# Performance work log

Hardware: AMD Instinct MI355X
Metric: run time of the kernel (lower is better)

Reference implementation:

```python
import jax, jax.numpy as jnp
import numpy as np
import math

LMAX = 10
N_SH = (LMAX + 1) ** 2  # 121
_lambert_sh_k = [3.1415926535897927, 2.0943951023931957, 0.7853981633974483, 0.0,
                 -0.13089969389957473, 0.0, 0.04908738521234052, 0.0,
                 -0.024543692606170262, 0.0, 0.014317154020265985]
_reps = [2 * l + 1 for l in range(LMAX + 1)]
LAMBERT_VEC = jnp.asarray(np.repeat(np.array(_lambert_sh_k, np.float32), _reps))  # (121,)
EXPO_VEC = jnp.asarray(np.repeat(np.array([l * (l + 1) / 2.0 for l in range(LMAX + 1)], np.float32), _reps))  # (121,)

def _dfact(n):
    # double factorial n!!, with (-1)!! = 1
    out = 1.0
    while n > 0:
        out *= n
        n -= 2
    return out

def _K(l, m):
    return math.sqrt((2 * l + 1) / (4 * math.pi) * math.factorial(l - m) / math.factorial(l + m))

def sh_basis(d):
    """Real spherical harmonics up to LMAX, e3nn-style ordering (m=-l..l per l),
    'integral' normalization, homogeneous in |d| (normalize=False semantics: Y_l(r*u)=r^l Y_l(u))."""
    r = jnp.linalg.norm(d, axis=-1, keepdims=True)  # (N,1)
    u = d / jnp.maximum(r, 1e-12)
    x, y, z = u[..., 0], u[..., 1], u[..., 2]
    rr = r[..., 0]
    # c[m] = sin^m(theta)*cos(m*phi), s[m] = sin^m(theta)*sin(m*phi) via complex power recurrence
    c = [jnp.ones_like(x)]
    s = [jnp.zeros_like(x)]
    for m in range(1, LMAX + 1):
        c.append(x * c[m - 1] - y * s[m - 1])
        s.append(x * s[m - 1] + y * c[m - 1])
    # Q[l][m] = P_l^m(z) / sin^m(theta) (polynomial in z, no Condon-Shortley)
    Q = {}
    for m in range(LMAX + 1):
        Q[(m, m)] = jnp.full_like(x, _dfact(2 * m - 1))
        if m < LMAX:
            Q[(m + 1, m)] = (2 * m + 1) * z * Q[(m, m)]
        for l in range(m + 2, LMAX + 1):
            Q[(l, m)] = ((2 * l - 1) * z * Q[(l - 1, m)] - (l + m - 1) * Q[(l - 2, m)]) / (l - m)
    cols = [None] * N_SH
    for l in range(LMAX + 1):
        rl = rr ** l
        cols[l * l + l] = _K(l, 0) * Q[(l, 0)] * rl
        for m in range(1, l + 1):
            f = math.sqrt(2.0) * _K(l, m)
            cols[l * l + l + m] = f * Q[(l, m)] * c[m] * rl
            cols[l * l + l - m] = f * Q[(l, m)] * s[m] * rl
    return jnp.stack(cols, axis=-1)  # (N, 121)

def setup_inputs() -> dict:
    key = jax.random.key(0)
    ks = jax.random.split(key, 16)
    N = 131072
    W = 512
    normals = jax.random.normal(ks[0], (N, 3), jnp.float32)
    normals = normals / jnp.linalg.norm(normals, axis=-1, keepdims=True)
    view_dirs = jax.random.normal(ks[1], (N, 3), jnp.float32)
    view_dirs = view_dirs / jnp.linalg.norm(view_dirs, axis=-1, keepdims=True)
    feature = jax.random.normal(ks[2], (N, 16), jnp.float32)
    ref_SH = jax.random.normal(ks[3], (N, N_SH, 3), jnp.float32) * 0.1
    def xavier(k, fi, fo):
        lim = math.sqrt(6.0 / (fi + fo))
        return jax.random.uniform(k, (fi, fo), jnp.float32, -lim, lim)
    return {
        'normals': normals, 'view_dirs': view_dirs, 'feature': feature, 'ref_SH': ref_SH,
        'w0': xavier(ks[4], 8, W), 'b0': jnp.zeros((W,), jnp.float32),
        'w1': xavier(ks[5], W, W), 'b1': jnp.zeros((W,), jnp.float32),
        'w2': xavier(ks[6], W, W), 'b2': jnp.zeros((W,), jnp.float32),
        'w3': xavier(ks[7], W, W), 'b3': jnp.zeros((W,), jnp.float32),
        'wc': xavier(ks[8], W, 27), 'bc': jnp.zeros((27,), jnp.float32),
    }

def reference(normals, view_dirs, feature, ref_SH, w0, b0, w1, b1, w2, b2, w3, b3, wc, bc):
    roughness = jax.nn.softplus(feature[..., 0:1])          # (N,1)
    coe = feature[..., 1:10]                                 # (N,9)
    albedo = jax.nn.sigmoid(feature[..., 10:13])             # (N,3)
    spec = jax.nn.sigmoid(feature[..., 13:16])               # (N,3)
    # diffuse irradiance: Lambert-coefficient-weighted SH of normals
    irradiance = jax.nn.relu(jnp.einsum('nk,nkc->nc', sh_basis(normals) * LAMBERT_VEC, ref_SH))
    diffuse = albedo * irradiance
    # specular: roughness-filtered SH of reflection direction
    dot = jnp.sum(normals * view_dirs, axis=-1, keepdims=True)  # (N,1)
    wr = 2.0 * normals * dot - view_dirs                        # (N,3)
    decay = jnp.exp(-EXPO_VEC * roughness)                      # (N,121)
    light = jax.nn.relu(jnp.einsum('nk,nkc->nc', sh_basis(wr) * decay, ref_SH))
    # conditioning MLP
    h = jnp.concatenate([dot, view_dirs, normals, roughness], axis=-1)  # (N,8)
    h = jax.nn.relu(h @ w0 + b0)
    h = jax.nn.relu(h @ w1 + b1)
    h = jax.nn.relu(h @ w2 + b2)
    h = jax.nn.relu(h @ w3 + b3)
    cs = h @ wc + bc                                            # (N,27)
    rr_ = jnp.sum(cs[..., 0:9] * coe, axis=-1, keepdims=True)
    gg_ = jnp.sum(cs[..., 9:18] * coe, axis=-1, keepdims=True)
    bb_ = jnp.sum(cs[..., 18:27] * coe, axis=-1, keepdims=True)
    gate = jax.nn.sigmoid(jnp.concatenate([rr_, gg_, bb_], axis=-1))  # (N,3)
    specular = spec * light * gate
    raw_rgb = diffuse + specular
    sh_light = jnp.concatenate([light, irradiance], axis=0)     # (2N,3)
    return raw_rgb, albedo, diffuse, specular, sh_light
```

## Files before the change

### kernel.cpp

```cpp
#include <hip/hip_runtime.h>
#include <hip/hip_bf16.h>
#include <stdint.h>
#include <math.h>

typedef __hip_bfloat16 bf16;
typedef __attribute__((ext_vector_type(8))) __bf16 bf16x8;
typedef __attribute__((ext_vector_type(4))) float f32x4;

__device__ __forceinline__ float b2f(bf16 x){ return __bfloat162float(x); }
__device__ __forceinline__ bf16 f2b(float x){ return __float2bfloat16(x); }
__device__ __forceinline__ float sigmoidf_(float x){ return 1.f/(1.f+expf(-x)); }

__device__ __forceinline__ void ld_lds16(const void* g, void* l){
  __builtin_amdgcn_global_load_lds(
      (const __attribute__((address_space(1))) uint32_t*)g,
      (__attribute__((address_space(3))) uint32_t*)l, 16, 0, 0);
}

__device__ const float DTAB[11] = {1.f,1.f,3.f,15.f,105.f,945.f,10395.f,135135.f,
                                   2027025.f,34459425.f,654729075.f};
__device__ const float LAMB[11] = {3.1415926535897927f, 2.0943951023931957f, 0.7853981633974483f,
                                   0.0f, -0.13089969389957473f, 0.0f, 0.04908738521234052f, 0.0f,
                                   -0.024543692606170262f, 0.0f, 0.014317154020265985f};

__global__ __launch_bounds__(256) void transpose512(const float* __restrict__ w1,
                                                    const float* __restrict__ w2,
                                                    const float* __restrict__ w3,
                                                    bf16* __restrict__ outT){
  __shared__ float tile[64][65];
  const float* src = (blockIdx.z==0) ? w1 : (blockIdx.z==1) ? w2 : w3;
  bf16* dst = outT + (size_t)blockIdx.z*512*512;
  int bx = blockIdx.x*64, by = blockIdx.y*64;
  int tx = threadIdx.x & 63, tg = threadIdx.x >> 6;
  #pragma unroll
  for (int rr=0; rr<16; rr++){
    int row = tg*16 + rr;
    tile[row][tx] = src[(by+row)*512 + bx+tx];
  }
  __syncthreads();
  #pragma unroll
  for (int rr=0; rr<16; rr++){
    int row = tg*16 + rr;
    dst[(size_t)(bx+row)*512 + by+tx] = f2b(tile[tx][row]);
  }
}

__global__ __launch_bounds__(256) void prep_wcT(const float* __restrict__ wc, bf16* __restrict__ wcT){
  int i = blockIdx.x*256 + threadIdx.x;
  int n = i >> 9, k = i & 511;
  wcT[i] = f2b((n < 27) ? wc[k*27 + n] : 0.f);
}

__global__ __launch_bounds__(256) void prep_small(const float* b0, const float* b1,
    const float* b2, const float* b3, const float* bc, const float* w0,
    float* __restrict__ fsm){
  int i = blockIdx.x*256 + threadIdx.x;
  if (i >= 6176) return;
  float v;
  if (i < 512)       v = b0[i];
  else if (i < 1024) v = b1[i-512];
  else if (i < 1536) v = b2[i-1024];
  else if (i < 2048) v = b3[i-1536];
  else if (i < 2080){ int j=i-2048; v = (j<27) ? bc[j] : 0.f; }
  else               v = w0[i-2080];
  fsm[i] = v;
}

__global__ __launch_bounds__(256) void point_kernel(
    const float* __restrict__ nrm, const float* __restrict__ vwd,
    const float* __restrict__ feat, const float* __restrict__ refsh,
    float* __restrict__ out, float* __restrict__ lightirr, float* __restrict__ h0, int N)
{
  __shared__ float rows[32*363];
  __shared__ float s_klm[66];
  const int tid = threadIdx.x;
  if (tid < 66){
    int l = 0, t = tid;
    while (t >= l+1){ t -= (l+1); l++; }
    int m = t;
    double fr = 1.0;
    for (int i = l-m+1; i <= l+m; i++) fr /= (double)i;
    double K = sqrt((2.0*l+1.0)/(4.0*3.14159265358979323846) * fr);
    if (m > 0) K *= 1.4142135623730951;
    s_klm[tid] = (float)K;
  }
  const int wave = tid >> 6, lane = tid & 63;
  const long p0 = (long)blockIdx.x * 32;
  const float* gbase = refsh + p0*363;
  #pragma unroll
  for (int t=0; t<12; t++){
    int fi = t*1024 + wave*256 + lane*4;
    if (fi < 32*363)
      ld_lds16(gbase + fi, rows + t*1024 + wave*256);
  }
  __syncthreads();

  const int r = tid >> 3, j = tid & 7;
  const long p = p0 + r;
  const float* row = rows + r*363;

  float nx=nrm[p*3+0], ny=nrm[p*3+1], nz=nrm[p*3+2];
  float vx=vwd[p*3+0], vy=vwd[p*3+1], vz=vwd[p*3+2];
  float f0 = feat[p*16];
  float rough = (f0 > 20.f) ? f0 : log1pf(expf(f0));
  float dotnv = nx*vx + ny*vy + nz*vz;
  float wx = 2.f*nx*dotnv - vx, wy = 2.f*ny*dotnv - vy, wz = 2.f*nz*dotnv - vz;

  float rA = sqrtf(nx*nx+ny*ny+nz*nz);
  float iA = 1.f/fmaxf(rA, 1e-12f);
  float ax = nx*iA, ay = ny*iA, az = nz*iA;
  float rB = sqrtf(wx*wx+wy*wy+wz*wz);
  float iB = 1.f/fmaxf(rB, 1e-12f);
  float bx = wx*iB, by = wy*iB, bz = wz*iB;

  float irr[3] = {0,0,0}, lig[3] = {0,0,0};
  const float E = expf(-rough);

  auto process_m = [&](int m){
    float cmA=1.f, smA=0.f, cmB=1.f, smB=0.f, rmA=1.f, rmB=1.f;
    for (int mm=1; mm<=m; mm++){
      float tA = ax*cmA - ay*smA; smA = ax*smA + ay*cmA; cmA = tA;
      float tB = bx*cmB - by*smB; smB = bx*smB + by*cmB; cmB = tB;
      rmA *= rA; rmB *= rB;
    }
    float qA = DTAB[m], qB = DTAB[m], pA = 0.f, pB = 0.f;
    float rlA = rmA, rlB = rmB;
    float dec = expf(-0.5f*(float)(m*(m+1))*rough);
    float e   = expf(-(float)(m+1)*rough);
    for (int l=m; l<=10; l++){
      if (l > m){
        float nA, nB;
        if (l == m+1){ nA = (float)(2*m+1)*az*qA; nB = (float)(2*m+1)*bz*qB; }
        else {
          float inv = 1.f/(float)(l-m);
          nA = ((float)(2*l-1)*az*qA - (float)(l+m-1)*pA)*inv;
          nB = ((float)(2*l-1)*bz*qB - (float)(l+m-1)*pB)*inv;
        }
        pA = qA; qA = nA; pB = qB; qB = nB;
        rlA *= rA; rlB *= rB;
        dec *= e; e *= E;
      }
      float kc = s_klm[l*(l+1)/2 + m];
      float wI = kc*qA*rlA*LAMB[l];
      float wL = kc*qB*rlB*dec;
      int k0 = l*l + l;
      if (m == 0){
        const float* rp = row + k0*3;
        #pragma unroll
        for (int c=0;c<3;c++){ float rv = rp[c]; irr[c] += wI*rv; lig[c] += wL*rv; }
      } else {
        const float* rpp = row + (k0+m)*3;
        const float* rpm = row + (k0-m)*3;
        #pragma unroll
        for (int c=0;c<3;c++){ float rv = rpp[c]; irr[c] += wI*cmA*rv; lig[c] += wL*cmB*rv; }
        #pragma unroll
        for (int c=0;c<3;c++){ float rv = rpm[c]; irr[c] += wI*smA*rv; lig[c] += wL*smB*rv; }
      }
    }
  };
  process_m(j);
  if (j < 3) process_m(j+8);

  #pragma unroll
  for (int c=0;c<3;c++){
    #pragma unroll
    for (int s=4; s>=1; s>>=1){
      irr[c] += __shfl_xor(irr[c], s);
      lig[c] += __shfl_xor(lig[c], s);
    }
  }
  float ir[3], lg[3];
  #pragma unroll
  for (int c=0;c<3;c++){ ir[c] = fmaxf(irr[c],0.f); lg[c] = fmaxf(lig[c],0.f); }

  long N3 = (long)3*N;
  if (j < 3){
    int c = j;
    float alb = sigmoidf_(feat[p*16+10+c]);
    out[N3   + p*3 + c] = alb;
    out[2*N3 + p*3 + c] = alb*ir[c];
    out[4*N3 + p*3 + c] = lg[c];
    out[4*N3 + ((long)N+p)*3 + c] = ir[c];
  }
  if (j < 6) lightirr[p*6 + j] = (j<3) ? lg[j] : ir[j-3];
  float hv = (j==0)?dotnv : (j==1)?vx : (j==2)?vy : (j==3)?vz :
             (j==4)?nx   : (j==5)?ny : (j==6)?nz : rough;
  h0[p*8 + j] = hv;
}

__global__ __launch_bounds__(256) void gemm0(const float* __restrict__ h0,
    const float* __restrict__ w0f, const float* __restrict__ b0f,
    bf16* __restrict__ outp, int rows){
  __shared__ float w0s[8*512];
  __shared__ float b0s[512];
  int tid = threadIdx.x;
  #pragma unroll
  for (int i=0;i<16;i++){ int e = i*256+tid; w0s[e] = w0f[e]; }
  b0s[tid] = b0f[tid]; b0s[256+tid] = b0f[256+tid];
  __syncthreads();
  long r = (long)blockIdx.x*32 + (tid>>3);
  int cg = tid & 7;
  float hv[8];
  #pragma unroll
  for (int k=0;k<8;k++) hv[k] = h0[r*8+k];
  bf16* orow = outp + r*512;
  for (int cc=0; cc<64; cc++){
    int col = cg + cc*8;
    float a = b0s[col];
    #pragma unroll
    for (int k=0;k<8;k++) a += hv[k]*w0s[k*512+col];
    orow[col] = f2b(fmaxf(a, 0.f));
  }
}

template<int WN, bool RELU, bool OUTBF>
__global__ __launch_bounds__(256) void gemm_bt(
    const bf16* __restrict__ A, const bf16* __restrict__ Bt,
    const float* __restrict__ bias,
    void* __restrict__ outv, int ldout, int rows)
{
  constexpr int BN = 32*WN;
  constexpr int BK = 64;
  constexpr int NCH_B = BN/32;
  __shared__ bf16 As[128*BK];
  __shared__ bf16 Bs[BN*BK];
  const int tid  = threadIdx.x;
  const int wave = tid >> 6, lane = tid & 63;
  const int quad = lane >> 4, l16 = lane & 15;
  const int wrow = wave >> 1, wcol = wave & 1;
  const int m_off = wrow*64, n_off = wcol*16*WN;
  const long rowBase = (long)blockIdx.x * 128;
  const int  colBase = blockIdx.y * BN;

  f32x4 acc[4][WN];
  #pragma unroll
  for (int i=0;i<4;i++)
    #pragma unroll
    for (int j=0;j<WN;j++) acc[i][j] = (f32x4){0.f,0.f,0.f,0.f};

  for (int kt=0; kt<512; kt+=BK){
    #pragma unroll
    for (int ch=0; ch<4; ch++){
      int flat = ch*2048 + wave*512 + lane*8;
      int m = flat >> 6, kk = flat & 63;
      ld_lds16(A + (rowBase + m)*512 + kt + kk, As + ch*2048 + wave*512);
    }
    #pragma unroll
    for (int ch=0; ch<NCH_B; ch++){
      int flat = ch*2048 + wave*512 + lane*8;
      int n = flat >> 6, kk = flat & 63;
      ld_lds16(Bt + (long)(colBase + n)*512 + kt + kk, Bs + ch*2048 + wave*512);
    }
    __syncthreads();
    #pragma unroll
    for (int kk=0; kk<BK; kk+=32){
      bf16x8 af[4], bfr[WN];
      #pragma unroll
      for (int i=0;i<4;i++)
        af[i] = *(const bf16x8*)(As + (m_off + i*16 + l16)*BK + kk + quad*8);
      #pragma unroll
      for (int j=0;j<WN;j++)
        bfr[j] = *(const bf16x8*)(Bs + (n_off + j*16 + l16)*BK + kk + quad*8);
      #pragma unroll
      for (int i=0;i<4;i++)
        #pragma unroll
        for (int j=0;j<WN;j++)
          acc[i][j] = __builtin_amdgcn_mfma_f32_16x16x32_bf16(af[i], bfr[j], acc[i][j], 0,0,0);
    }
    __syncthreads();
  }
  #pragma unroll
  for (int j=0;j<WN;j++){
    int cg = colBase + n_off + j*16 + l16;
    float bv = bias[cg];
    #pragma unroll
    for (int i=0;i<4;i++){
      long rg0 = rowBase + m_off + i*16 + quad*4;
      #pragma unroll
      for (int r=0;r<4;r++){
        float v = acc[i][j][r] + bv;
        if (RELU) v = fmaxf(v, 0.f);
        if (OUTBF) ((bf16*)outv)[(rg0+r)*(long)ldout + cg] = f2b(v);
        else       ((float*)outv)[(rg0+r)*(long)ldout + cg] = v;
      }
    }
  }
}

__global__ __launch_bounds__(256) void epilogue_kernel(const float* __restrict__ cs,
    const float* __restrict__ feat, const float* __restrict__ lightirr,
    float* __restrict__ out, long base, int N, int rows){
  int t = blockIdx.x*256 + threadIdx.x;
  if (t >= rows) return;
  long gp = base + t;
  const float* c = cs + (long)t*32;
  const float* f = feat + gp*16;
  float rr=0.f, gg=0.f, bb=0.f;
  #pragma unroll
  for (int j=0;j<9;j++){
    float co = f[1+j];
    rr += c[j]*co; gg += c[9+j]*co; bb += c[18+j]*co;
  }
  float gate[3] = { sigmoidf_(rr), sigmoidf_(gg), sigmoidf_(bb) };
  const float* li = lightirr + gp*6;
  long N3 = (long)3*N;
  #pragma unroll
  for (int cc=0; cc<3; cc++){
    float spec = sigmoidf_(f[13+cc]);
    float alb  = sigmoidf_(f[10+cc]);
    float specular = spec * li[cc] * gate[cc];
    float diffuse  = alb * li[3+cc];
    out[gp*3 + cc]        = diffuse + specular;
    out[3*N3 + gp*3 + cc] = specular;
  }
}

extern "C" void kernel_launch(void* const* d_in, const int* in_sizes, int n_in,
                              void* d_out, int out_size, void* d_ws, size_t ws_size,
                              hipStream_t stream) {
  const float* normals = (const float*)d_in[0];
  const float* viewd   = (const float*)d_in[1];
  const float* feat    = (const float*)d_in[2];
  const float* refsh   = (const float*)d_in[3];
  float* out = (float*)d_out;
  int N = in_sizes[0] / 3;

  char* ws = (char*)d_ws;
  size_t off = 0;
  bf16* wT  = (bf16*)(ws + off);            off += (size_t)3*512*512*2;
  bf16* wcT = (bf16*)(ws + off);            off += (size_t)32*512*2;
  float* fsm = (float*)(ws + off);          off += (size_t)6176*4; off = (off+255)&~(size_t)255;
  float* h0 = (float*)(ws + off);           off += (size_t)N*8*4;
  float* lightirr = (float*)(ws + off);     off += (size_t)N*6*4;
  size_t fixed = off;

  size_t avail = (ws_size > fixed) ? (ws_size - fixed) : 0;
  long chunk = (long)(avail / 2176) & ~255L;
  if (chunk < 256) chunk = 256;
  if (chunk > N) chunk = N;
  bf16* hA = (bf16*)(ws + fixed);
  bf16* hB = (bf16*)(ws + fixed + (size_t)chunk*1024);
  float* cs = (float*)(ws + fixed + (size_t)chunk*2048);

  transpose512<<<dim3(8,8,3), 256, 0, stream>>>((const float*)d_in[6], (const float*)d_in[8],
                                                (const float*)d_in[10], wT);
  prep_wcT<<<64, 256, 0, stream>>>((const float*)d_in[12], wcT);
  prep_small<<<25, 256, 0, stream>>>((const float*)d_in[5], (const float*)d_in[7],
                                     (const float*)d_in[9], (const float*)d_in[11],
                                     (const float*)d_in[13], (const float*)d_in[4], fsm);
  point_kernel<<<N/32, 256, 0, stream>>>(normals, viewd, feat, refsh, out, lightirr, h0, N);

  for (long base = 0; base < N; base += chunk){
    long rows = (N - base < chunk) ? (N - base) : chunk;
    gemm0<<<rows/32, 256, 0, stream>>>(h0 + base*8, fsm + 2080, fsm + 0, hA, (int)rows);
    gemm_bt<4,true,true ><<<dim3(rows/128,4), 256, 0, stream>>>(hA, wT,          fsm + 512,  hB, 512, (int)rows);
    gemm_bt<4,true,true ><<<dim3(rows/128,4), 256, 0, stream>>>(hB, wT + 262144, fsm + 1024, hA, 512, (int)rows);
    gemm_bt<4,true,true ><<<dim3(rows/128,4), 256, 0, stream>>>(hA, wT + 524288, fsm + 1536, hB, 512, (int)rows);
    gemm_bt<1,false,false><<<dim3(rows/128,1), 256, 0, stream>>>(hB, wcT,        fsm + 2048, cs,  32, (int)rows);
    epilogue_kernel<<<rows/256, 256, 0, stream>>>(cs, feat, lightirr, out, base, N, (int)rows);
  }
}
```

Before: 801.6 us.

## Swizzle LDS layout in GEMMs and fuse head GEMM with gate epilogue

```diff
diff --git a/kernel.cpp b/kernel.cpp
--- a/kernel.cpp
+++ b/kernel.cpp
@@ -213,64 +213,63 @@
   }
 }
 
-template<int WN, bool RELU, bool OUTBF>
+
 __global__ __launch_bounds__(256) void gemm_bt(
     const bf16* __restrict__ A, const bf16* __restrict__ Bt,
-    const float* __restrict__ bias,
-    void* __restrict__ outv, int ldout, int rows)
+    const float* __restrict__ bias, bf16* __restrict__ outp, int rows)
 {
-  constexpr int BN = 32*WN;
   constexpr int BK = 64;
-  constexpr int NCH_B = BN/32;
   __shared__ bf16 As[128*BK];
-  __shared__ bf16 Bs[BN*BK];
+  __shared__ bf16 Bs[128*BK];
   const int tid  = threadIdx.x;
   const int wave = tid >> 6, lane = tid & 63;
   const int quad = lane >> 4, l16 = lane & 15;
   const int wrow = wave >> 1, wcol = wave & 1;
-  const int m_off = wrow*64, n_off = wcol*16*WN;
+  const int m_off = wrow*64, n_off = wcol*64;
   const long rowBase = (long)blockIdx.x * 128;
-  const int  colBase = blockIdx.y * BN;
-
-  f32x4 acc[4][WN];
+  const int  colBase = blockIdx.y * 128;
+  const int sw = (lane&7) ^ ((lane>>3)&7);
+  const int rowlow = lane >> 3;
+
+  f32x4 acc[4][4];
   #pragma unroll
   for (int i=0;i<4;i++)
     #pragma unroll
-    for (int j=0;j<WN;j++) acc[i][j] = (f32x4){0.f,0.f,0.f,0.f};
+    for (int j=0;j<4;j++) acc[i][j] = (f32x4){0.f,0.f,0.f,0.f};
 
   for (int kt=0; kt<512; kt+=BK){
     #pragma unroll
     for (int ch=0; ch<4; ch++){
-      int flat = ch*2048 + wave*512 + lane*8;
-      int m = flat >> 6, kk = flat & 63;
-      ld_lds16(A + (rowBase + m)*512 + kt + kk, As + ch*2048 + wave*512);
-    }
-    #pragma unroll
-    for (int ch=0; ch<NCH_B; ch++){
-      int flat = ch*2048 + wave*512 + lane*8;
-      int n = flat >> 6, kk = flat & 63;
-      ld_lds16(Bt + (long)(colBase + n)*512 + kt + kk, Bs + ch*2048 + wave*512);
+      int m = ch*32 + wave*8 + rowlow;
+      ld_lds16(A + (rowBase + m)*512 + kt + sw*8, As + ch*2048 + wave*512);
+      int n = ch*32 + wave*8 + rowlow;
+      ld_lds16(Bt + (long)(colBase + n)*512 + kt + sw*8, Bs + ch*2048 + wave*512);
     }
     __syncthreads();
     #pragma unroll
     for (int kk=0; kk<BK; kk+=32){
-      bf16x8 af[4], bfr[WN];
-      #pragma unroll
-      for (int i=0;i<4;i++)
-        af[i] = *(const bf16x8*)(As + (m_off + i*16 + l16)*BK + kk + quad*8);
-      #pragma unroll
-      for (int j=0;j<WN;j++)
-        bfr[j] = *(const bf16x8*)(Bs + (n_off + j*16 + l16)*BK + kk + quad*8);
+      const int kb = kk >> 3;
+      bf16x8 af[4], bfr[4];
+      #pragma unroll
+      for (int i=0;i<4;i++){
+        int row = m_off + i*16 + l16;
+        af[i] = *(const bf16x8*)(As + row*BK + (((kb+quad) ^ (row&7))<<3));
+      }
+      #pragma unroll
+      for (int j=0;j<4;j++){
+        int row = n_off + j*16 + l16;
+        bfr[j] = *(const bf16x8*)(Bs + row*BK + (((kb+quad) ^ (row&7))<<3));
+      }
       #pragma unroll
       for (int i=0;i<4;i++)
         #pragma unroll
-        for (int j=0;j<WN;j++)
+        for (int j=0;j<4;j++)
           acc[i][j] = __builtin_amdgcn_mfma_f32_16x16x32_bf16(af[i], bfr[j], acc[i][j], 0,0,0);
     }
     __syncthreads();
   }
   #pragma unroll
-  for (int j=0;j<WN;j++){
+  for (int j=0;j<4;j++){
     int cg = colBase + n_off + j*16 + l16;
     float bv = bias[cg];
     #pragma unroll
@@ -278,40 +277,99 @@
       long rg0 = rowBase + m_off + i*16 + quad*4;
       #pragma unroll
       for (int r=0;r<4;r++){
-        float v = acc[i][j][r] + bv;
-        if (RELU) v = fmaxf(v, 0.f);
-        if (OUTBF) ((bf16*)outv)[(rg0+r)*(long)ldout + cg] = f2b(v);
-        else       ((float*)outv)[(rg0+r)*(long)ldout + cg] = v;
-      }
-    }
-  }
-}
-
-__global__ __launch_bounds__(256) void epilogue_kernel(const float* __restrict__ cs,
+        float v = fmaxf(acc[i][j][r] + bv, 0.f);
+        outp[(rg0+r)*512 + cg] = f2b(v);
+      }
+    }
+  }
+}
+
+__global__ __launch_bounds__(256) void head_gate(
+    const bf16* __restrict__ A, const bf16* __restrict__ wcT,
+    const float* __restrict__ bcp,
     const float* __restrict__ feat, const float* __restrict__ lightirr,
-    float* __restrict__ out, long base, int N, int rows){
-  int t = blockIdx.x*256 + threadIdx.x;
-  if (t >= rows) return;
-  long gp = base + t;
-  const float* c = cs + (long)t*32;
-  const float* f = feat + gp*16;
-  float rr=0.f, gg=0.f, bb=0.f;
-  #pragma unroll
-  for (int j=0;j<9;j++){
-    float co = f[1+j];
-    rr += c[j]*co; gg += c[9+j]*co; bb += c[18+j]*co;
-  }
-  float gate[3] = { sigmoidf_(rr), sigmoidf_(gg), sigmoidf_(bb) };
-  const float* li = lightirr + gp*6;
-  long N3 = (long)3*N;
-  #pragma unroll
-  for (int cc=0; cc<3; cc++){
-    float spec = sigmoidf_(f[13+cc]);
-    float alb  = sigmoidf_(f[10+cc]);
-    float specular = spec * li[cc] * gate[cc];
-    float diffuse  = alb * li[3+cc];
-    out[gp*3 + cc]        = diffuse + specular;
-    out[3*N3 + gp*3 + cc] = specular;
+    float* __restrict__ out, long base, int N)
+{
+  constexpr int BK = 64;
+  __shared__ bf16 As[128*BK];
+  __shared__ bf16 Bs[32*BK];
+  __shared__ float scs[128*33];
+  const int tid  = threadIdx.x;
+  const int wave = tid >> 6, lane = tid & 63;
+  const int quad = lane >> 4, l16 = lane & 15;
+  const int wrow = wave >> 1, wcol = wave & 1;
+  const int m_off = wrow*64, n_off = wcol*16;
+  const long rowBase = (long)blockIdx.x * 128;
+  const int sw = (lane&7) ^ ((lane>>3)&7);
+  const int rowlow = lane >> 3;
+
+  f32x4 acc[4];
+  #pragma unroll
+  for (int i=0;i<4;i++) acc[i] = (f32x4){0.f,0.f,0.f,0.f};
+
+  for (int kt=0; kt<512; kt+=BK){
+    #pragma unroll
+    for (int ch=0; ch<4; ch++){
+      int m = ch*32 + wave*8 + rowlow;
+      ld_lds16(A + (rowBase + m)*512 + kt + sw*8, As + ch*2048 + wave*512);
+    }
+    {
+      int n = wave*8 + rowlow;
+      ld_lds16(wcT + (long)n*512 + kt + sw*8, Bs + wave*512);
+    }
+    __syncthreads();
+    #pragma unroll
+    for (int kk=0; kk<BK; kk+=32){
+      const int kb = kk >> 3;
+      bf16x8 af[4], bfr;
+      #pragma unroll
+      for (int i=0;i<4;i++){
+        int row = m_off + i*16 + l16;
+        af[i] = *(const bf16x8*)(As + row*BK + (((kb+quad) ^ (row&7))<<3));
+      }
+      {
+        int row = n_off + l16;
+        bfr = *(const bf16x8*)(Bs + row*BK + (((kb+quad) ^ (row&7))<<3));
+      }
+      #pragma unroll
+      for (int i=0;i<4;i++)
+        acc[i] = __builtin_amdgcn_mfma_f32_16x16x32_bf16(af[i], bfr, acc[i], 0,0,0);
+    }
+    __syncthreads();
+  }
+  {
+    int cg = n_off + l16;
+    float bv = bcp[cg];
+    #pragma unroll
+    for (int i=0;i<4;i++){
+      int r0 = m_off + i*16 + quad*4;
+      #pragma unroll
+      for (int r=0;r<4;r++)
+        scs[(r0+r)*33 + cg] = acc[i][r] + bv;
+    }
+  }
+  __syncthreads();
+  if (tid < 128){
+    long gp = base + rowBase + tid;
+    const float* f = feat + gp*16;
+    const float* c = scs + tid*33;
+    float rr=0.f, gg=0.f, bb=0.f;
+    #pragma unroll
+    for (int j=0;j<9;j++){
+      float co = f[1+j];
+      rr += c[j]*co; gg += c[9+j]*co; bb += c[18+j]*co;
+    }
+    float gate[3] = { sigmoidf_(rr), sigmoidf_(gg), sigmoidf_(bb) };
+    const float* li = lightirr + gp*6;
+    long N3 = (long)3*N;
+    #pragma unroll
+    for (int cc=0; cc<3; cc++){
+      float spec = sigmoidf_(f[13+cc]);
+      float alb  = sigmoidf_(f[10+cc]);
+      float specular = spec * li[cc] * gate[cc];
+      out[gp*3 + cc]        = alb*li[3+cc] + specular;
+      out[3*N3 + gp*3 + cc] = specular;
+    }
   }
 }
 
@@ -335,12 +393,11 @@
   size_t fixed = off;
 
   size_t avail = (ws_size > fixed) ? (ws_size - fixed) : 0;
-  long chunk = (long)(avail / 2176) & ~255L;
+  long chunk = (long)(avail / 2048) & ~255L;
   if (chunk < 256) chunk = 256;
   if (chunk > N) chunk = N;
   bf16* hA = (bf16*)(ws + fixed);
   bf16* hB = (bf16*)(ws + fixed + (size_t)chunk*1024);
-  float* cs = (float*)(ws + fixed + (size_t)chunk*2048);
 
   transpose512<<<dim3(8,8,3), 256, 0, stream>>>((const float*)d_in[6], (const float*)d_in[8],
                                                 (const float*)d_in[10], wT);
@@ -353,10 +410,9 @@
   for (long base = 0; base < N; base += chunk){
     long rows = (N - base < chunk) ? (N - base) : chunk;
     gemm0<<<rows/32, 256, 0, stream>>>(h0 + base*8, fsm + 2080, fsm + 0, hA, (int)rows);
-    gemm_bt<4,true,true ><<<dim3(rows/128,4), 256, 0, stream>>>(hA, wT,          fsm + 512,  hB, 512, (int)rows);
-    gemm_bt<4,true,true ><<<dim3(rows/128,4), 256, 0, stream>>>(hB, wT + 262144, fsm + 1024, hA, 512, (int)rows);
-    gemm_bt<4,true,true ><<<dim3(rows/128,4), 256, 0, stream>>>(hA, wT + 524288, fsm + 1536, hB, 512, (int)rows);
-    gemm_bt<1,false,false><<<dim3(rows/128,1), 256, 0, stream>>>(hB, wcT,        fsm + 2048, cs,  32, (int)rows);
-    epilogue_kernel<<<rows/256, 256, 0, stream>>>(cs, feat, lightirr, out, base, N, (int)rows);
-  }
-}
+    gemm_bt<<<dim3(rows/128,4), 256, 0, stream>>>(hA, wT,          fsm + 512,  hB, (int)rows);
+    gemm_bt<<<dim3(rows/128,4), 256, 0, stream>>>(hB, wT + 262144, fsm + 1024, hA, (int)rows);
+    gemm_bt<<<dim3(rows/128,4), 256, 0, stream>>>(hA, wT + 524288, fsm + 1536, hB, (int)rows);
+    head_gate<<<rows/128, 256, 0, stream>>>(hB, wcT, fsm + 2048, feat, lightirr, out, base, N);
+  }
+}
```

New measurement: 765.2 us. -4.5%, faster.
